# Kernel tuning notes

Hardware: AMD Instinct MI355X
Metric: run time of the kernel (lower is better)

## Reference

```python
import jax, jax.numpy as jnp
import numpy as np
from functools import partial

DN = ('NCHW', 'OIHW', 'NCHW')

def conv2d(x, w, b, stride):
    y = jax.lax.conv_general_dilated(x, w, (stride, stride), 'VALID', dimension_numbers=DN)
    return y + b[None, :, None, None]

def squash(s, eps=1e-8):
    norm = jnp.linalg.norm(s, axis=-1, keepdims=True)
    return (norm ** 2 / (1 + norm ** 2)) * s / (norm + eps)

def setup_inputs() -> dict:
    key = jax.random.key(0)
    ks = jax.random.split(key, 10)
    B, H, W = 16, 32, 512
    F, CAPS, E, OD = 64, 8, 8, 16
    H1 = (H - 6) // 2 + 1          # 14
    W1 = (W - 6) // 2 + 1          # 254
    N = F * H1 * W1 // CAPS        # 28448
    s = 0.05
    return {
        'x': jax.random.normal(ks[0], (B, H, W), jnp.float32),
        'conv1_w': jax.random.normal(ks[1], (F, 1, 6, 6), jnp.float32) * s,
        'conv1_b': jnp.zeros((F,), jnp.float32),
        'conv2_w': jax.random.normal(ks[2], (F, F, 6, 6), jnp.float32) * s,
        'conv2_b': jnp.zeros((F,), jnp.float32),
        'conv3_w': jax.random.normal(ks[3], (F, 2 * F, 1, 1), jnp.float32) * s,
        'conv3_b': jnp.zeros((F,), jnp.float32),
        'pc_w': jax.random.normal(ks[4], (N, CAPS, CAPS), jnp.float32) * s,  # [N, in, out]
        'pc_b': jnp.zeros((N, CAPS), jnp.float32),
        'ec_w': jax.random.normal(ks[5], (N, E, OD, CAPS), jnp.float32),
    }

def reference(x, conv1_w, conv1_b, conv2_w, conv2_b, conv3_w, conv3_b, pc_w, pc_b, ec_w):
    CAPS = pc_w.shape[1]
    NUM_ITER = 3
    B = x.shape[0]
    h = x[:, None]                                  # [B,1,H,W]
    h = jax.nn.relu(conv2d(h, conv1_w, conv1_b, 2)) # [B,F,14,254]
    y = jnp.pad(h, ((0, 0), (0, 0), (2, 3), (2, 3)))  # ZeroPad2d((2,3,2,3))
    y = jax.nn.relu(conv2d(y, conv2_w, conv2_b, 1))
    h = jax.nn.relu(jnp.concatenate((h, y), axis=1))
    h = conv2d(h, conv3_w, conv3_b, 1)              # [B,F,14,254]
    u_in = h.reshape(B, -1, CAPS)                   # [B,N,caps_len]
    # PrimaryCaps: N independent Linear(caps,caps) -> one batched einsum
    u = jnp.einsum('bni,nio->bno', u_in, pc_w) + pc_b[None]
    # EmotionCaps: per-capsule prediction u_hat [B,N,E,out_dim]
    u_hat = jnp.einsum('neoi,bni->bneo', ec_w, u)
    N, E = ec_w.shape[0], ec_w.shape[1]
    b_log = jnp.zeros((B, N, E), u_hat.dtype)
    v = None
    for r in range(NUM_ITER):
        c = jax.nn.softmax(b_log, axis=2)           # [B,N,E]
        s = jnp.einsum('bne,bneo->beo', c, u_hat)   # [B,E,out_dim]
        v = squash(s)
        if r < NUM_ITER - 1:
            b_log = b_log + jnp.einsum('bneo,beo->bne', u_hat, v)
    return jnp.linalg.norm(v, axis=-1)              # [B,E]
```

## Files before the change

### kernel.cpp

```cpp
#include <hip/hip_runtime.h>
#include <hip/hip_bf16.h>
#include <math.h>

#define BB 16
#define H1 14
#define W1 254
#define HPH 19
#define HPW2 264
#define NCAP 28448
#define FLATSZ 227584

typedef __attribute__((ext_vector_type(8))) short bf16x8;
typedef __attribute__((ext_vector_type(4))) float f32x4;

__device__ __forceinline__ ushort f2bf(float f) {
  __hip_bfloat16 h = __float2bfloat16(f);
  return *(ushort*)&h;
}

__global__ __launch_bounds__(256) void prep_w(const float* __restrict__ w2, const float* __restrict__ w3,
                                              ushort* __restrict__ wb, float* __restrict__ w3t) {
  int idx = blockIdx.x * 256 + threadIdx.x;
  if (idx < 147456) {
    int co = idx / 2304; int rem = idx - co * 2304;
    int tap = rem >> 6; int ci = rem & 63;
    wb[idx] = f2bf(w2[(co * 64 + ci) * 36 + tap]);
  }
  if (idx < 8192) {
    int co = idx & 63; int c = idx >> 6;
    w3t[idx] = w3[co * 128 + c];
  }
}

__global__ __launch_bounds__(256) void conv1_k(const float* __restrict__ x, const float* __restrict__ w1,
                                               const float* __restrict__ b1, float* __restrict__ hc) {
  const int i = blockIdx.x, b = blockIdx.y;
  __shared__ float xs[6 * 512];
  __shared__ float wsh[2304];
  __shared__ float bsh[64];
  const int t = threadIdx.x;
  for (int idx = t; idx < 6 * 512; idx += 256) {
    int r = idx >> 9, c = idx & 511;
    xs[idx] = x[((size_t)b * 32 + 2 * i + r) * 512 + c];
  }
  for (int idx = t; idx < 2304; idx += 256) wsh[idx] = w1[idx];
  if (t < 64) bsh[t] = b1[t];
  __syncthreads();
  if (t < 254) {
    for (int c = 0; c < 64; c++) {
      float acc = bsh[c];
#pragma unroll
      for (int p = 0; p < 6; p++)
#pragma unroll
        for (int q = 0; q < 6; q++)
          acc = fmaf(xs[p * 512 + 2 * t + q], wsh[c * 36 + p * 6 + q], acc);
      acc = fmaxf(acc, 0.f);
      hc[(((size_t)b * 64 + c) * H1 + i) * W1 + t] = acc;
    }
  }
}

__global__ __launch_bounds__(256) void nhwc_k(const float* __restrict__ hc, ushort* __restrict__ hpc) {
  const int ct = blockIdx.x, i = blockIdx.y, b = blockIdx.z;
  const int c0 = ct * 64;
  __shared__ float ls[64 * 65];
  const int t = threadIdx.x;
  for (int idx = t; idx < 4096; idx += 256) {
    int ci = idx >> 6, cc = idx & 63;
    int c = c0 + cc;
    ls[ci * 65 + cc] = (c < W1) ? hc[(((size_t)b * 64 + ci) * H1 + i) * W1 + c] : 0.f;
  }
  __syncthreads();
  uint* outp = (uint*)hpc;
  for (int idx = t; idx < 2048; idx += 256) {
    int cc = idx >> 5, ci2 = idx & 31;
    int c = c0 + cc;
    if (c < W1) {
      float f0 = ls[(2 * ci2) * 65 + cc];
      float f1 = ls[(2 * ci2 + 1) * 65 + cc];
      uint pk = (uint)f2bf(f0) | ((uint)f2bf(f1) << 16);
      outp[(((size_t)b * HPH + 2 + i) * HPW2 + 2 + c) * 32 + ci2] = pk;
    }
  }
}

__device__ __forceinline__ void stage_b(const ushort* __restrict__ wb, ushort* __restrict__ bbuf,
                                        int tap, int w, int l) {
#pragma unroll
  for (int r = 0; r < 2; r++) {
    int v = r * 256 + w * 64 + l;
    int co = v >> 3, s = v & 7;
    int g = s ^ (co & 7);
    const ushort* gp = wb + co * 2304 + tap * 64 + g * 8;
    ushort* lp = bbuf + (size_t)(r * 256 + w * 64) * 8;
    __builtin_amdgcn_global_load_lds((const uint*)gp, (uint*)lp, 16, 0, 0);
  }
}

__global__ __launch_bounds__(256, 1) void conv2_mfma(const ushort* __restrict__ hpc,
                                                     const ushort* __restrict__ wb,
                                                     const float* __restrict__ b2, float* __restrict__ y) {
  const int b = blockIdx.z, i = blockIdx.y, j0 = blockIdx.x * 128;
  const int t = threadIdx.x;
  const int w = t >> 6, l = t & 63;
  const int lr = l & 15, quad = l >> 4;

  __shared__ ushort bls[2][4096];

  f32x4 acc[2][4];
#pragma unroll
  for (int mt = 0; mt < 2; mt++)
#pragma unroll
    for (int nt = 0; nt < 4; nt++) acc[mt][nt] = (f32x4){0.f, 0.f, 0.f, 0.f};

  const ushort* abase = hpc + (((size_t)b * HPH + i) * HPW2 + (j0 + w * 32 + lr)) * 64 + quad * 8;

  bf16x8 a0[2][2], a1[2][2];

#define ALOAD(dst, tap)                                                        \
  {                                                                            \
    const int p_ = (tap) / 6, q_ = (tap) % 6;                                  \
    const ushort* ap_ = abase + ((size_t)p_ * HPW2 + q_) * 64;                 \
    dst[0][0] = *(const bf16x8*)(ap_);                                         \
    dst[0][1] = *(const bf16x8*)(ap_ + 1024);                                  \
    dst[1][0] = *(const bf16x8*)(ap_ + 32);                                    \
    dst[1][1] = *(const bf16x8*)(ap_ + 32 + 1024);                             \
  }

#define COMPUTE(a, bp)                                                         \
  {                                                                            \
    _Pragma("unroll")                                                          \
    for (int ch = 0; ch < 2; ch++) {                                           \
      const int g2 = ch * 4 + quad;                                            \
      _Pragma("unroll")                                                        \
      for (int nt = 0; nt < 4; nt++) {                                         \
        const int co = nt * 16 + lr;                                           \
        bf16x8 bf = *(const bf16x8*)((bp) + co * 64 + ((g2 ^ (co & 7)) * 8));  \
        acc[0][nt] = __builtin_amdgcn_mfma_f32_16x16x32_bf16(a[ch][0], bf, acc[0][nt], 0, 0, 0); \
        acc[1][nt] = __builtin_amdgcn_mfma_f32_16x16x32_bf16(a[ch][1], bf, acc[1][nt], 0, 0, 0); \
      }                                                                        \
    }                                                                          \
  }

  stage_b(wb, &bls[0][0], 0, w, l);
  __syncthreads();
  ALOAD(a0, 0);

  for (int tp = 0; tp < 36; tp += 2) {
    stage_b(wb, &bls[1][0], tp + 1, w, l);
    ALOAD(a1, tp + 1);
    COMPUTE(a0, &bls[0][0]);
    __syncthreads();
    if (tp + 2 < 36) {
      stage_b(wb, &bls[0][0], tp + 2, w, l);
      ALOAD(a0, tp + 2);
    }
    COMPUTE(a1, &bls[1][0]);
    __syncthreads();
  }

#pragma unroll
  for (int nt = 0; nt < 4; nt++) {
    const int co = nt * 16 + lr;
    const float bias = b2[co];
    float* yrow = y + (((size_t)b * 64 + co) * H1 + i) * W1;
#pragma unroll
    for (int mt = 0; mt < 2; mt++) {
      const int jb = j0 + w * 32 + mt * 16 + quad * 4;
#pragma unroll
      for (int r = 0; r < 4; r++) {
        int j = jb + r;
        if (j < W1) yrow[j] = fmaxf(acc[mt][nt][r] + bias, 0.f);
      }
    }
  }
#undef ALOAD
#undef COMPUTE
}

__global__ __launch_bounds__(256) void conv3_k(const float* __restrict__ hc, const float* __restrict__ y,
                                               const float* __restrict__ w3t, const float* __restrict__ b3,
                                               float* __restrict__ out3) {
  const int b = blockIdx.z, i = blockIdx.y, j0 = blockIdx.x * 64;
  __shared__ float cs[32][64];
  __shared__ float wsh[32][64];
  const int t = threadIdx.x;
  const int cog = t >> 4, jg = t & 15;
  float acc[4][4];
#pragma unroll
  for (int a = 0; a < 4; a++)
#pragma unroll
    for (int j = 0; j < 4; j++) acc[a][j] = 0.f;

  for (int ch = 0; ch < 4; ch++) {
    __syncthreads();
    for (int idx = t; idx < 2048; idx += 256) {
      int cl = idx >> 6; int j = j0 + (idx & 63);
      int c = ch * 32 + cl;
      float v = 0.f;
      if (j < W1) {
        if (c < 64) v = hc[(((size_t)b * 64 + c) * H1 + i) * W1 + j];
        else        v = y[(((size_t)b * 64 + (c - 64)) * H1 + i) * W1 + j];
      }
      cs[cl][idx & 63] = v;
    }
    for (int idx = t; idx < 2048; idx += 256)
      wsh[idx >> 6][idx & 63] = w3t[(ch * 32 + (idx >> 6)) * 64 + (idx & 63)];
    __syncthreads();
#pragma unroll
    for (int c = 0; c < 32; c++) {
      float4 xv = *(const float4*)&cs[c][jg * 4];
      float4 wv = *(const float4*)&wsh[c][cog * 4];
#pragma unroll
      for (int jj = 0; jj < 4; jj++) {
        float xx = (&xv.x)[jj];
        acc[0][jj] = fmaf(wv.x, xx, acc[0][jj]);
        acc[1][jj] = fmaf(wv.y, xx, acc[1][jj]);
        acc[2][jj] = fmaf(wv.z, xx, acc[2][jj]);
        acc[3][jj] = fmaf(wv.w, xx, acc[3][jj]);
      }
    }
  }
#pragma unroll
  for (int a = 0; a < 4; a++) {
    int co = cog * 4 + a;
    float bias = b3[co];
#pragma unroll
    for (int jj = 0; jj < 4; jj++) {
      int j = j0 + jg * 4 + jj;
      if (j < W1) out3[(((size_t)b * 64 + co) * H1 + i) * W1 + j] = acc[a][jj] + bias;
    }
  }
}

__global__ __launch_bounds__(256) void pc_k(const float* __restrict__ out3, const float* __restrict__ pcw,
                                            const float* __restrict__ pcb, float* __restrict__ u) {
  int n = blockIdx.x * 256 + threadIdx.x;
  if (n >= NCAP) return;
  float pw[64];
  const float4* pwp = (const float4*)(pcw + (size_t)n * 64);
#pragma unroll
  for (int k = 0; k < 16; k++) {
    float4 v = pwp[k];
    pw[4 * k] = v.x; pw[4 * k + 1] = v.y; pw[4 * k + 2] = v.z; pw[4 * k + 3] = v.w;
  }
  float pb[8];
  {
    const float4* pbp = (const float4*)(pcb + (size_t)n * 8);
    float4 a = pbp[0], b = pbp[1];
    pb[0] = a.x; pb[1] = a.y; pb[2] = a.z; pb[3] = a.w;
    pb[4] = b.x; pb[5] = b.y; pb[6] = b.z; pb[7] = b.w;
  }
  for (int b = 0; b < BB; b++) {
    const float4* uip = (const float4*)(out3 + (size_t)b * FLATSZ + (size_t)n * 8);
    float4 a = uip[0], c = uip[1];
    float ui[8] = {a.x, a.y, a.z, a.w, c.x, c.y, c.z, c.w};
    float uo[8];
#pragma unroll
    for (int o = 0; o < 8; o++) uo[o] = pb[o];
#pragma unroll
    for (int i2 = 0; i2 < 8; i2++)
#pragma unroll
      for (int o = 0; o < 8; o++) uo[o] = fmaf(ui[i2], pw[i2 * 8 + o], uo[o]);
    float4* up = (float4*)(u + ((size_t)b * NCAP + n) * 8);
    up[0] = make_float4(uo[0], uo[1], uo[2], uo[3]);
    up[1] = make_float4(uo[4], uo[5], uo[6], uo[7]);
  }
}

template <int CTRL>
__device__ __forceinline__ float dpp_add(float x) {
  int y = __builtin_amdgcn_update_dpp(0, __float_as_int(x), CTRL, 0xF, 0xF, true);
  return x + __int_as_float(y);
}

template <int MODE>
__global__ __launch_bounds__(256, 8) void route4_k(const float* __restrict__ u, const float* __restrict__ ecw,
                                                   const float* __restrict__ v, float* __restrict__ sout) {
  __shared__ float red[4096];
  __shared__ float vlds[1024];
  float* us = red;

  const int t = threadIdx.x, l = t & 63, wv = t >> 6;
  const int b0 = blockIdx.y * 8;
  const int n0 = blockIdx.x * 32 + wv * 8;
  const int xaddr = (l ^ 32) << 2;

  if (MODE) {
    for (int idx = t; idx < 1024; idx += 256) vlds[idx] = v[b0 * 128 + idx];
  }
#pragma unroll
  for (int bb = 0; bb < 8; bb++)
    us[wv * 512 + bb * 64 + l] = u[((size_t)(b0 + bb) * NCAP + n0) * 8 + l];
  if (MODE) __syncthreads();

  float sacc[16];
#pragma unroll
  for (int k = 0; k < 16; k++) sacc[k] = 0.f;

  const float4* ebase = (const float4*)(ecw + (size_t)n0 * 1024) + (l << 2);

#pragma unroll 1
  for (int nn = 0; nn < 8; nn++) {
    const float4* ep = ebase + (size_t)nn * 64;
    const float4 e0 = ep[0], e1 = ep[1], e2 = ep[2], e3 = ep[3];
    const float ec[16] = {e0.x, e0.y, e0.z, e0.w, e1.x, e1.y, e1.z, e1.w,
                          e2.x, e2.y, e2.z, e2.w, e3.x, e3.y, e3.z, e3.w};
#pragma unroll
    for (int bb = 0; bb < 8; bb++) {
      const float4* up = (const float4*)&us[wv * 512 + bb * 64 + nn * 8];
      const float4 ua = up[0], ub = up[1];
      const float uv[8] = {ua.x, ua.y, ua.z, ua.w, ub.x, ub.y, ub.z, ub.w};
      float h0 = 0.f, h1 = 0.f;
#pragma unroll
      for (int k = 0; k < 8; k++) {
        h0 = fmaf(ec[k], uv[k], h0);
        h1 = fmaf(ec[8 + k], uv[k], h1);
      }
      if (MODE == 0) {
        sacc[2 * bb] += h0;
        sacc[2 * bb + 1] += h1;
      } else {
        const float2 vv = *(const float2*)&vlds[bb * 128 + 2 * l];
        float p = fmaf(h0, vv.x, h1 * vv.y);
        p = dpp_add<0xB1>(p);
        p = dpp_add<0x4E>(p);
        p = dpp_add<0x141>(p);
        const float ex = __expf(p);
        float den = dpp_add<0x140>(ex);
        den += __int_as_float(__builtin_amdgcn_ds_swizzle(__float_as_int(den), 0x401F));
        den += __int_as_float(__builtin_amdgcn_ds_bpermute(xaddr, __float_as_int(den)));
        const float cc = ex * __builtin_amdgcn_rcpf(den);
        sacc[2 * bb] = fmaf(cc, h0, sacc[2 * bb]);
        sacc[2 * bb + 1] = fmaf(cc, h1, sacc[2 * bb + 1]);
      }
    }
  }

  __syncthreads();
#pragma unroll
  for (int k = 0; k < 16; k++) red[k * 256 + wv * 64 + l] = sacc[k];
  __syncthreads();
#pragma unroll
  for (int m = 0; m < 4; m++) {
    int slot = t + 256 * m;
    int bl = slot >> 7, eo = slot & 127;
    int k = 2 * bl + (eo & 1), l2 = eo >> 1;
    const float* r = red + k * 256 + l2;
    atomicAdd(&sout[(b0 + bl) * 128 + eo], r[0] + r[64] + r[128] + r[192]);
  }
}

__global__ void squash_k(const float* __restrict__ s, float scale, const float* __restrict__ vprev,
                         float* __restrict__ vout) {
  int t = threadIdx.x;
  const float* sp = s + t * 16;
  float sv[16]; float nn = 0.f;
#pragma unroll
  for (int o = 0; o < 16; o++) { float x = sp[o] * scale; sv[o] = x; nn = fmaf(x, x, nn); }
  float norm = sqrtf(nn);
  float f = nn / (1.f + nn) / (norm + 1e-8f);
#pragma unroll
  for (int o = 0; o < 16; o++) {
    float base = vprev ? vprev[t * 16 + o] : 0.f;
    vout[t * 16 + o] = base + f * sv[o];
  }
}

__global__ void squash_out_k(const float* __restrict__ s, float* __restrict__ out) {
  int t = threadIdx.x;
  float nn = 0.f;
#pragma unroll
  for (int o = 0; o < 16; o++) { float x = s[t * 16 + o]; nn = fmaf(x, x, nn); }
  float norm = sqrtf(nn);
  float f = nn / (1.f + nn) / (norm + 1e-8f);
  out[t] = f * norm;
}

extern "C" void kernel_launch(void* const* d_in, const int* in_sizes, int n_in,
                              void* d_out, int out_size, void* d_ws, size_t ws_size,
                              hipStream_t stream) {
  const float* x   = (const float*)d_in[0];
  const float* w1  = (const float*)d_in[1];
  const float* b1  = (const float*)d_in[2];
  const float* w2  = (const float*)d_in[3];
  const float* b2  = (const float*)d_in[4];
  const float* w3  = (const float*)d_in[5];
  const float* b3  = (const float*)d_in[6];
  const float* pcw = (const float*)d_in[7];
  const float* pcb = (const float*)d_in[8];
  const float* ecw = (const float*)d_in[9];
  float* out = (float*)d_out;

  float* ws = (float*)d_ws;
  size_t o = 0;
  float* hc   = ws + o; o += 3641344;
  float* yb   = ws + o; o += 3641344;
  float* out3 = ws + o; o += 3641344;
  ushort* hpc = (ushort*)(ws + o); o += 2568192;
  ushort* wb  = (ushort*)(ws + o); o += 73728;
  float* w3t  = ws + o; o += 8192;
  float* s0   = ws + o; o += 2048;
  float* s1   = ws + o; o += 2048;
  float* s2   = ws + o; o += 2048;
  float* v0   = ws + o; o += 2048;
  float* v1   = ws + o; o += 2048;
  float* ub   = hc;

  hipMemsetAsync(hpc, 0, (size_t)16 * HPH * HPW2 * 64 * 2, stream);
  hipMemsetAsync(s0, 0, 3 * 2048 * 4, stream);

  prep_w<<<576, 256, 0, stream>>>(w2, w3, wb, w3t);
  conv1_k<<<dim3(14, 16), 256, 0, stream>>>(x, w1, b1, hc);
  nhwc_k<<<dim3(4, 14, 16), 256, 0, stream>>>(hc, hpc);
  conv2_mfma<<<dim3(2, 14, 16), 256, 0, stream>>>(hpc, wb, b2, yb);
  conv3_k<<<dim3(4, 14, 16), 256, 0, stream>>>(hc, yb, w3t, b3, out3);
  pc_k<<<112, 256, 0, stream>>>(out3, pcw, pcb, ub);

  route4_k<0><<<dim3(889, 2), 256, 0, stream>>>(ub, ecw, nullptr, s0);
  squash_k<<<1, 128, 0, stream>>>(s0, 0.125f, nullptr, v0);
  route4_k<1><<<dim3(889, 2), 256, 0, stream>>>(ub, ecw, v0, s1);
  squash_k<<<1, 128, 0, stream>>>(s1, 1.0f, v0, v1);
  route4_k<1><<<dim3(889, 2), 256, 0, stream>>>(ub, ecw, v1, s2);
  squash_out_k<<<1, 128, 0, stream>>>(s2, out);
}
```

Measured before the change: 543.7 us.

## Convert routing weights to fp16 once and double-buffer their loads in routing

A new kernel converts the 116 MB fp32 emotion-capsule weight tensor to packed fp16 at the start of every call. The three routing passes then read half the bytes. The routing loop now prefetches the next capsule's weights while it processes the current one, and the occupancy hint is lowered from 8 to 4 to leave room for the extra registers. The conversion itself reads all the fp32 weights and writes the fp16 copy each call, and fp16 round-toward-zero adds precision error to the predictions.

```diff
diff --git a/kernel.cpp b/kernel.cpp
--- a/kernel.cpp
+++ b/kernel.cpp
@@ -12,6 +12,8 @@
 
 typedef __attribute__((ext_vector_type(8))) short bf16x8;
 typedef __attribute__((ext_vector_type(4))) float f32x4;
+typedef __attribute__((ext_vector_type(2))) __fp16 f16x2;
+typedef __attribute__((ext_vector_type(4))) uint uint4v;
 
 __device__ __forceinline__ ushort f2bf(float f) {
   __hip_bfloat16 h = __float2bfloat16(f);
@@ -30,6 +32,18 @@
     int co = idx & 63; int c = idx >> 6;
     w3t[idx] = w3[co * 128 + c];
   }
+}
+
+__global__ __launch_bounds__(256) void cvt_ec(const float* __restrict__ ecw, uint* __restrict__ ech) {
+  size_t i = (size_t)blockIdx.x * 256 + threadIdx.x;
+  const float4* s = (const float4*)ecw + i * 2;
+  float4 a = s[0], b = s[1];
+  uint4v pk;
+  { f16x2 h = __builtin_amdgcn_cvt_pkrtz(a.x, a.y); pk.x = *(uint*)&h; }
+  { f16x2 h = __builtin_amdgcn_cvt_pkrtz(a.z, a.w); pk.y = *(uint*)&h; }
+  { f16x2 h = __builtin_amdgcn_cvt_pkrtz(b.x, b.y); pk.z = *(uint*)&h; }
+  { f16x2 h = __builtin_amdgcn_cvt_pkrtz(b.z, b.w); pk.w = *(uint*)&h; }
+  *((uint4v*)ech + i) = pk;
 }
 
 __global__ __launch_bounds__(256) void conv1_k(const float* __restrict__ x, const float* __restrict__ w1,
@@ -275,7 +289,7 @@
 }
 
 template <int MODE>
-__global__ __launch_bounds__(256, 8) void route4_k(const float* __restrict__ u, const float* __restrict__ ecw,
+__global__ __launch_bounds__(256, 4) void route5_k(const float* __restrict__ u, const uint* __restrict__ ech,
                                                    const float* __restrict__ v, float* __restrict__ sout) {
   __shared__ float red[4096];
   __shared__ float vlds[1024];
@@ -298,14 +312,18 @@
 #pragma unroll
   for (int k = 0; k < 16; k++) sacc[k] = 0.f;
 
-  const float4* ebase = (const float4*)(ecw + (size_t)n0 * 1024) + (l << 2);
-
-#pragma unroll 1
-  for (int nn = 0; nn < 8; nn++) {
-    const float4* ep = ebase + (size_t)nn * 64;
-    const float4 e0 = ep[0], e1 = ep[1], e2 = ep[2], e3 = ep[3];
-    const float ec[16] = {e0.x, e0.y, e0.z, e0.w, e1.x, e1.y, e1.z, e1.w,
-                          e2.x, e2.y, e2.z, e2.w, e3.x, e3.y, e3.z, e3.w};
+  const uint4v* hbase = (const uint4v*)(ech + (size_t)n0 * 512) + (l * 2);
+
+  auto proc = [&](int nn, uint4v w0, uint4v w1) {
+    float ec[16];
+#pragma unroll
+    for (int k = 0; k < 4; k++) {
+      uint t0 = w0[k], t1 = w1[k];
+      f16x2 a = *(f16x2*)&t0;
+      f16x2 b = *(f16x2*)&t1;
+      ec[2 * k]     = (float)a.x; ec[2 * k + 1] = (float)a.y;
+      ec[8 + 2 * k] = (float)b.x; ec[8 + 2 * k + 1] = (float)b.y;
+    }
 #pragma unroll
     for (int bb = 0; bb < 8; bb++) {
       const float4* up = (const float4*)&us[wv * 512 + bb * 64 + nn * 8];
@@ -335,6 +353,19 @@
         sacc[2 * bb + 1] = fmaf(cc, h1, sacc[2 * bb + 1]);
       }
     }
+  };
+
+  uint4v ca0 = hbase[0], ca1 = hbase[1];
+#pragma unroll 1
+  for (int nn = 0; nn < 8; nn += 2) {
+    const uint4v* pb = hbase + (size_t)(nn + 1) * 128;
+    uint4v cb0 = pb[0], cb1 = pb[1];
+    proc(nn, ca0, ca1);
+    if (nn + 2 < 8) {
+      const uint4v* pa = hbase + (size_t)(nn + 2) * 128;
+      ca0 = pa[0]; ca1 = pa[1];
+    }
+    proc(nn + 1, cb0, cb1);
   }
 
   __syncthreads();
@@ -405,22 +436,24 @@
   float* s2   = ws + o; o += 2048;
   float* v0   = ws + o; o += 2048;
   float* v1   = ws + o; o += 2048;
+  uint* ech   = (uint*)(ws + o); o += 14565376;
   float* ub   = hc;
 
   hipMemsetAsync(hpc, 0, (size_t)16 * HPH * HPW2 * 64 * 2, stream);
   hipMemsetAsync(s0, 0, 3 * 2048 * 4, stream);
 
   prep_w<<<576, 256, 0, stream>>>(w2, w3, wb, w3t);
+  cvt_ec<<<14224, 256, 0, stream>>>(ecw, ech);
   conv1_k<<<dim3(14, 16), 256, 0, stream>>>(x, w1, b1, hc);
   nhwc_k<<<dim3(4, 14, 16), 256, 0, stream>>>(hc, hpc);
   conv2_mfma<<<dim3(2, 14, 16), 256, 0, stream>>>(hpc, wb, b2, yb);
   conv3_k<<<dim3(4, 14, 16), 256, 0, stream>>>(hc, yb, w3t, b3, out3);
   pc_k<<<112, 256, 0, stream>>>(out3, pcw, pcb, ub);
 
-  route4_k<0><<<dim3(889, 2), 256, 0, stream>>>(ub, ecw, nullptr, s0);
+  route5_k<0><<<dim3(889, 2), 256, 0, stream>>>(ub, ech, nullptr, s0);
   squash_k<<<1, 128, 0, stream>>>(s0, 0.125f, nullptr, v0);
-  route4_k<1><<<dim3(889, 2), 256, 0, stream>>>(ub, ecw, v0, s1);
+  route5_k<1><<<dim3(889, 2), 256, 0, stream>>>(ub, ech, v0, s1);
   squash_k<<<1, 128, 0, stream>>>(s1, 1.0f, v0, v1);
-  route4_k<1><<<dim3(889, 2), 256, 0, stream>>>(ub, ecw, v1, s2);
+  route5_k<1><<<dim3(889, 2), 256, 0, stream>>>(ub, ech, v1, s2);
   squash_out_k<<<1, 128, 0, stream>>>(s2, out);
 }
```

Result: faster. 478.1 us (-12.1%).
